# Kernel tuning notes

Hardware: AMD Instinct MI355X
Metric: run time of the kernel (lower is better)

The kernel has to match this reference:

```python
import jax, jax.numpy as jnp
import numpy as np

H = 512        # num_hidden
Z = 512        # latent_len
TIME = 0.2
N_STEPS = 4    # fixed-step RK4 replaces adaptive dopri5 (same dynamics math)
B, N = 4, 4096


def _linear_params(k, fin, fout):
    k1, k2 = jax.random.split(k)
    s = 1.0 / np.sqrt(fin)
    W = jax.random.uniform(k1, (fout, fin), minval=-s, maxval=s, dtype=jnp.float32)
    b = jax.random.uniform(k2, (fout,), minval=-s, maxval=s, dtype=jnp.float32)
    return W, b


def setup_inputs() -> dict:
    key = jax.random.key(0)
    ks = jax.random.split(key, 16)
    inp = {
        "code": jax.random.normal(ks[0], (B, 1, Z), dtype=jnp.float32),
        "x": jax.random.uniform(ks[1], (B, N, 3), dtype=jnp.float32),
    }
    dims = {"l1": (3, H), "l2": (H, H), "l3": (H, H), "l4": (H, 3), "cond": (Z, H)}
    i = 2
    for f in ("f1", "f2"):
        for name, (fin, fout) in dims.items():
            W, b = _linear_params(ks[i], fin, fout)
            i += 1
            inp[f + "_" + name + "_w"] = W
            inp[f + "_" + name + "_b"] = b
    return inp


def _node_block(x, sf, W1, b1, W2, b2, W3, b3, W4, b4):
    """Fixed-step RK4 integration of ODEFunc dynamics over [0, TIME].
    x: (B,N,3) point state; sf: (B,1,H) precomputed tanh(cond(code)) shape features
    (constant along the trajectory since the latent code has zero dynamics)."""
    def dyn(p):
        pf = jax.nn.relu(p @ W1.T + b1)          # (B,N,H) point features
        h = pf * sf                               # gated point-shape features
        h = jax.nn.relu(h @ W2.T + b2) + h        # residual stage 1
        h = jax.nn.relu(h @ W3.T + b3) + h        # residual stage 2
        return jnp.tanh(h @ W4.T + b4)            # (B,N,3) flow direction

    dt = TIME / N_STEPS
    def step(p, _):
        k1 = dyn(p)
        k2 = dyn(p + 0.5 * dt * k1)
        k3 = dyn(p + 0.5 * dt * k2)
        k4 = dyn(p + dt * k3)
        return p + (dt / 6.0) * (k1 + 2.0 * k2 + 2.0 * k3 + k4), None

    x, _ = jax.lax.scan(step, x, None, length=N_STEPS)
    return x


def reference(code, x,
              f1_l1_w, f1_l1_b, f1_l2_w, f1_l2_b, f1_l3_w, f1_l3_b,
              f1_l4_w, f1_l4_b, f1_cond_w, f1_cond_b,
              f2_l1_w, f2_l1_b, f2_l2_w, f2_l2_b, f2_l3_w, f2_l3_b,
              f2_l4_w, f2_l4_b, f2_cond_w, f2_cond_b):
    sf1 = jnp.tanh(code @ f1_cond_w.T + f1_cond_b)  # (B,1,H), broadcasts over N
    x = _node_block(x, sf1, f1_l1_w, f1_l1_b, f1_l2_w, f1_l2_b,
                    f1_l3_w, f1_l3_b, f1_l4_w, f1_l4_b)
    sf2 = jnp.tanh(code @ f2_cond_w.T + f2_cond_b)
    x = _node_block(x, sf2, f2_l1_w, f2_l1_b, f2_l2_w, f2_l2_b,
                    f2_l3_w, f2_l3_b, f2_l4_w, f2_l4_b)
    return x  # pred_y: (B,N,3)
```

## Files before the change

### kernel.cpp

```cpp
#include <hip/hip_runtime.h>
#include <stdint.h>

typedef short short8 __attribute__((ext_vector_type(8)));
typedef float floatx16 __attribute__((ext_vector_type(16)));

#define NPTS 16384
#define TILE_M 64
#define THREADS 512
#define PA 4
#define PB 8

__device__ inline unsigned short f2bf(float f) {
  union { float f; unsigned u; } v; v.f = f;
  unsigned u = v.u;
  unsigned r = (u + 0x7fffu + ((u >> 16) & 1u)) >> 16;
  return (unsigned short)r;
}
__device__ inline float bf2f(unsigned short h) {
  union { unsigned u; float f; } v; v.u = ((unsigned)h) << 16;
  return v.f;
}

__global__ __launch_bounds__(THREADS, 2) void dyn_kernel(
    const float* __restrict__ p, const float* __restrict__ kprev, float cf,
    const unsigned short* __restrict__ w2f, const unsigned short* __restrict__ w3f,
    const float* __restrict__ sf, const float* __restrict__ w1,
    const float* __restrict__ b1, const float* __restrict__ b2,
    const float* __restrict__ b3, const float* __restrict__ w4,
    const float* __restrict__ b4, int update_mode, float* __restrict__ outp,
    const float* __restrict__ k1v, const float* __restrict__ k2v,
    const float* __restrict__ k3v, float dt6)
{
  __shared__ unsigned short act[TILE_M][520];
  __shared__ float pe[TILE_M][3];
  __shared__ float red[192][8];

  const int tid = threadIdx.x;
  const int wg = blockIdx.x;
  const int m0 = wg * TILE_M;
  const int batch = wg >> 6;
  const int lane = tid & 63;
  const int wid = tid >> 6;

  if (tid < TILE_M * 3) {
    int gi = m0 * 3 + tid;
    ((float*)pe)[tid] = p[gi] + cf * kprev[gi];
  }
  __syncthreads();

  {
    int j = tid;
    float ww0 = w1[j * 3 + 0], ww1 = w1[j * 3 + 1], ww2 = w1[j * 3 + 2];
    float bb = b1[j];
    float s = sf[batch * 512 + j];
    #pragma unroll 4
    for (int m = 0; m < TILE_M; ++m) {
      float v = fmaf(pe[m][0], ww0, fmaf(pe[m][1], ww1, fmaf(pe[m][2], ww2, bb)));
      v = fmaxf(v, 0.f) * s;
      act[m][j] = f2bf(v);
    }
  }
  __syncthreads();

  const int aBase = (lane & 31) * 1040 + (lane >> 5) * 16;
  const char* actB = (const char*)&act[0][0];
  const int bcol0 = (wid * 2 + 0) * 64 + lane;
  const int bcol1 = (wid * 2 + 1) * 64 + lane;

  for (int s = 0; s < 2; ++s) {
    const short8* bptr = (const short8*)(s ? w3f : w2f);
    const float* bias = s ? b3 : b2;
    const short8* bp0 = bptr + bcol0;
    const short8* bp1 = bptr + bcol1;
    floatx16 acc00{}, acc01{}, acc10{}, acc11{};

    short8 aq0[PA], aq1[PA], bq0[PB], bq1[PB];
    #pragma unroll
    for (int i = 0; i < PB - 1; ++i) {
      bq0[i] = bp0[i * 1024];
      bq1[i] = bp1[i * 1024];
    }
    #pragma unroll
    for (int i = 0; i < PA - 1; ++i) {
      aq0[i] = *(const short8*)(actB + aBase + i * 32);
      aq1[i] = *(const short8*)(actB + aBase + 33280 + i * 32);
    }

    #pragma unroll
    for (int kt = 0; kt < 32; ++kt) {
      int la = kt + PA - 1;
      if (la < 32) {
        aq0[la % PA] = *(const short8*)(actB + aBase + la * 32);
        aq1[la % PA] = *(const short8*)(actB + aBase + 33280 + la * 32);
      }
      int lb = kt + PB - 1;
      if (lb < 32) {
        bq0[lb % PB] = bp0[lb * 1024];
        bq1[lb % PB] = bp1[lb * 1024];
      }
      acc00 = __builtin_amdgcn_mfma_f32_32x32x16_bf16(aq0[kt % PA], bq0[kt % PB], acc00, 0, 0, 0);
      acc01 = __builtin_amdgcn_mfma_f32_32x32x16_bf16(aq0[kt % PA], bq1[kt % PB], acc01, 0, 0, 0);
      acc10 = __builtin_amdgcn_mfma_f32_32x32x16_bf16(aq1[kt % PA], bq0[kt % PB], acc10, 0, 0, 0);
      acc11 = __builtin_amdgcn_mfma_f32_32x32x16_bf16(aq1[kt % PA], bq1[kt % PB], acc11, 0, 0, 0);
    }

    __syncthreads();
    {
      int ncol0 = (wid * 2 + 0) * 32 + (lane & 31);
      int ncol1 = (wid * 2 + 1) * 32 + (lane & 31);
      float bs0 = bias[ncol0], bs1 = bias[ncol1];
      int rbase = 4 * (lane >> 5);
      #pragma unroll
      for (int reg = 0; reg < 16; ++reg) {
        int row = (reg & 3) + 8 * (reg >> 2) + rbase;
        float v = fmaxf(acc00[reg] + bs0, 0.f) + bf2f(act[row][ncol0]);
        act[row][ncol0] = f2bf(v);
        v = fmaxf(acc01[reg] + bs1, 0.f) + bf2f(act[row][ncol1]);
        act[row][ncol1] = f2bf(v);
        v = fmaxf(acc10[reg] + bs0, 0.f) + bf2f(act[32 + row][ncol0]);
        act[32 + row][ncol0] = f2bf(v);
        v = fmaxf(acc11[reg] + bs1, 0.f) + bf2f(act[32 + row][ncol1]);
        act[32 + row][ncol1] = f2bf(v);
      }
    }
    __syncthreads();
  }

  {
    int m = tid >> 3, jj = tid & 7;
    const unsigned short* arow = &act[m][0];
    float s0 = 0.f, s1 = 0.f, s2 = 0.f;
    #pragma unroll 8
    for (int kk = 0; kk < 64; ++kk) {
      int k = kk * 8 + jj;
      float a = bf2f(arow[k]);
      s0 = fmaf(a, w4[k], s0);
      s1 = fmaf(a, w4[512 + k], s1);
      s2 = fmaf(a, w4[1024 + k], s2);
    }
    red[m * 3 + 0][jj] = s0;
    red[m * 3 + 1][jj] = s1;
    red[m * 3 + 2][jj] = s2;
  }
  __syncthreads();
  if (tid < 192) {
    int mm = tid / 3, cc = tid % 3;
    float ssum = 0.f;
    #pragma unroll
    for (int q = 0; q < 8; ++q) ssum += red[tid][q];
    float flow = tanhf(ssum + b4[cc]);
    int gi = (m0 + mm) * 3 + cc;
    if (update_mode) {
      outp[gi] = p[gi] + dt6 * (k1v[gi] + 2.f * k2v[gi] + 2.f * k3v[gi] + flow);
    } else {
      outp[gi] = flow;
    }
  }
}

__global__ void setup_shuffle(const float* s0, const float* s1, const float* s2,
                              const float* s3, unsigned short* dst) {
  int idx = blockIdx.x * blockDim.x + threadIdx.x;
  int w = idx >> 15;
  int r = idx & 32767;
  int lane = r & 63;
  int tile = r >> 6;
  int nt = tile & 15, kt = tile >> 4;
  const float* W = (w == 0) ? s0 : (w == 1) ? s1 : (w == 2) ? s2 : s3;
  int n = nt * 32 + (lane & 31);
  int k0 = kt * 16 + (lane >> 5) * 8;
  const float* src = W + n * 512 + k0;
  unsigned short* d = dst + ((size_t)w << 18) + (size_t)r * 8;
  #pragma unroll
  for (int j = 0; j < 8; ++j) d[j] = f2bf(src[j]);
}

__global__ void setup_copy(const float* x, float* p) {
  int i = blockIdx.x * blockDim.x + threadIdx.x;
  if (i < NPTS * 3) p[i] = x[i];
}

__global__ void setup_sf(const float* code, const float* cw1, const float* cb1,
                         const float* cw2, const float* cb2, float* sfout) {
  int f = blockIdx.x >> 2, b = blockIdx.x & 3;
  const float* cw = f ? cw2 : cw1;
  const float* cb = f ? cb2 : cb1;
  int j = threadIdx.x;
  const float* c = code + b * 512;
  float s = cb[j];
  for (int k = 0; k < 512; ++k) s = fmaf(c[k], cw[j * 512 + k], s);
  sfout[f * 2048 + b * 512 + j] = tanhf(s);
}

extern "C" void kernel_launch(void* const* d_in, const int* in_sizes, int n_in,
                              void* d_out, int out_size, void* d_ws, size_t ws_size,
                              hipStream_t stream) {
  const float* code = (const float*)d_in[0];
  const float* x    = (const float*)d_in[1];
  char* ws = (char*)d_ws;
  float* p  = (float*)(ws);
  float* k1 = (float*)(ws + 196608);
  float* k2 = (float*)(ws + 2 * 196608);
  float* k3 = (float*)(ws + 3 * 196608);
  float* sf = (float*)(ws + 4 * 196608);
  unsigned short* wbf = (unsigned short*)(ws + 4 * 196608 + 16384);

  setup_shuffle<<<512, 256, 0, stream>>>((const float*)d_in[4], (const float*)d_in[6],
                                         (const float*)d_in[14], (const float*)d_in[16], wbf);
  setup_copy<<<192, 256, 0, stream>>>(x, p);
  setup_sf<<<8, 512, 0, stream>>>(code, (const float*)d_in[10], (const float*)d_in[11],
                                  (const float*)d_in[20], (const float*)d_in[21], sf);

  const float dt = 0.05f, dt6 = dt / 6.0f;
  float* out = (float*)d_out;
  for (int f = 0; f < 2; ++f) {
    const float* w1 = (const float*)d_in[2 + f * 10];
    const float* b1 = (const float*)d_in[3 + f * 10];
    const float* b2 = (const float*)d_in[5 + f * 10];
    const float* b3 = (const float*)d_in[7 + f * 10];
    const float* w4 = (const float*)d_in[8 + f * 10];
    const float* b4 = (const float*)d_in[9 + f * 10];
    const unsigned short* w2b = wbf + (f * 2 + 0) * 262144;
    const unsigned short* w3b = wbf + (f * 2 + 1) * 262144;
    const float* sff = sf + f * 2048;
    for (int st = 0; st < 4; ++st) {
      int last = (f == 1 && st == 3);
      dyn_kernel<<<256, THREADS, 0, stream>>>(p, p,  0.0f,      w2b, w3b, sff, w1, b1, b2, b3, w4, b4,
                                              0, k1, p, p, p, dt6);
      dyn_kernel<<<256, THREADS, 0, stream>>>(p, k1, 0.5f * dt, w2b, w3b, sff, w1, b1, b2, b3, w4, b4,
                                              0, k2, p, p, p, dt6);
      dyn_kernel<<<256, THREADS, 0, stream>>>(p, k2, 0.5f * dt, w2b, w3b, sff, w1, b1, b2, b3, w4, b4,
                                              0, k3, p, p, p, dt6);
      dyn_kernel<<<256, THREADS, 0, stream>>>(p, k3, dt,        w2b, w3b, sff, w1, b1, b2, b3, w4, b4,
                                              1, last ? out : p, k1, k2, k3, dt6);
    }
  }
}
```

Baseline: 942.6 us.

## Fuse all RK4 stages and both ODE blocks into one persistent kernel

Replaces the 32 per-stage kernel launches with a single kernel in which each workgroup keeps its 64-point tile's state, RK4 accumulator and stage input in shared memory and loops over both blocks, 4 steps and 4 stages. It also prefetches W2 fragments before the first-layer compute and replaces the shared-memory reduction for the output layer with wave shuffles. This removes launch overhead and the global round trips for p and k1..k3. The cost is that the grid stays at 256 workgroups for the whole run, so there is no inter-kernel overlap, and register pressure rises.

```diff
diff --git a/kernel.cpp b/kernel.cpp
--- a/kernel.cpp
+++ b/kernel.cpp
@@ -21,19 +21,20 @@
   return v.f;
 }
 
-__global__ __launch_bounds__(THREADS, 2) void dyn_kernel(
-    const float* __restrict__ p, const float* __restrict__ kprev, float cf,
-    const unsigned short* __restrict__ w2f, const unsigned short* __restrict__ w3f,
-    const float* __restrict__ sf, const float* __restrict__ w1,
-    const float* __restrict__ b1, const float* __restrict__ b2,
-    const float* __restrict__ b3, const float* __restrict__ w4,
-    const float* __restrict__ b4, int update_mode, float* __restrict__ outp,
-    const float* __restrict__ k1v, const float* __restrict__ k2v,
-    const float* __restrict__ k3v, float dt6)
+__global__ __launch_bounds__(THREADS, 2) void node_kernel(
+    const float* __restrict__ x, float* __restrict__ outp,
+    const unsigned short* __restrict__ wbf, const float* __restrict__ sfall,
+    const float* __restrict__ w1a, const float* __restrict__ b1a,
+    const float* __restrict__ b2a, const float* __restrict__ b3a,
+    const float* __restrict__ w4a, const float* __restrict__ b4a,
+    const float* __restrict__ w1b, const float* __restrict__ b1b,
+    const float* __restrict__ b2b, const float* __restrict__ b3b,
+    const float* __restrict__ w4b, const float* __restrict__ b4b)
 {
   __shared__ unsigned short act[TILE_M][520];
-  __shared__ float pe[TILE_M][3];
-  __shared__ float red[192][8];
+  __shared__ float pcur[TILE_M][3];
+  __shared__ float pev[TILE_M][3];
+  __shared__ float kac[TILE_M][3];
 
   const int tid = threadIdx.x;
   const int wg = blockIdx.x;
@@ -43,22 +44,9 @@
   const int wid = tid >> 6;
 
   if (tid < TILE_M * 3) {
-    int gi = m0 * 3 + tid;
-    ((float*)pe)[tid] = p[gi] + cf * kprev[gi];
-  }
-  __syncthreads();
-
-  {
-    int j = tid;
-    float ww0 = w1[j * 3 + 0], ww1 = w1[j * 3 + 1], ww2 = w1[j * 3 + 2];
-    float bb = b1[j];
-    float s = sf[batch * 512 + j];
-    #pragma unroll 4
-    for (int m = 0; m < TILE_M; ++m) {
-      float v = fmaf(pe[m][0], ww0, fmaf(pe[m][1], ww1, fmaf(pe[m][2], ww2, bb)));
-      v = fmaxf(v, 0.f) * s;
-      act[m][j] = f2bf(v);
-    }
+    float v = x[m0 * 3 + tid];
+    ((float*)pcur)[tid] = v;
+    ((float*)pev)[tid] = v;
   }
   __syncthreads();
 
@@ -67,95 +55,146 @@
   const int bcol0 = (wid * 2 + 0) * 64 + lane;
   const int bcol1 = (wid * 2 + 1) * 64 + lane;
 
-  for (int s = 0; s < 2; ++s) {
-    const short8* bptr = (const short8*)(s ? w3f : w2f);
-    const float* bias = s ? b3 : b2;
-    const short8* bp0 = bptr + bcol0;
-    const short8* bp1 = bptr + bcol1;
-    floatx16 acc00{}, acc01{}, acc10{}, acc11{};
-
-    short8 aq0[PA], aq1[PA], bq0[PB], bq1[PB];
-    #pragma unroll
-    for (int i = 0; i < PB - 1; ++i) {
-      bq0[i] = bp0[i * 1024];
-      bq1[i] = bp1[i * 1024];
-    }
-    #pragma unroll
-    for (int i = 0; i < PA - 1; ++i) {
-      aq0[i] = *(const short8*)(actB + aBase + i * 32);
-      aq1[i] = *(const short8*)(actB + aBase + 33280 + i * 32);
-    }
-
-    #pragma unroll
-    for (int kt = 0; kt < 32; ++kt) {
-      int la = kt + PA - 1;
-      if (la < 32) {
-        aq0[la % PA] = *(const short8*)(actB + aBase + la * 32);
-        aq1[la % PA] = *(const short8*)(actB + aBase + 33280 + la * 32);
-      }
-      int lb = kt + PB - 1;
-      if (lb < 32) {
-        bq0[lb % PB] = bp0[lb * 1024];
-        bq1[lb % PB] = bp1[lb * 1024];
-      }
-      acc00 = __builtin_amdgcn_mfma_f32_32x32x16_bf16(aq0[kt % PA], bq0[kt % PB], acc00, 0, 0, 0);
-      acc01 = __builtin_amdgcn_mfma_f32_32x32x16_bf16(aq0[kt % PA], bq1[kt % PB], acc01, 0, 0, 0);
-      acc10 = __builtin_amdgcn_mfma_f32_32x32x16_bf16(aq1[kt % PA], bq0[kt % PB], acc10, 0, 0, 0);
-      acc11 = __builtin_amdgcn_mfma_f32_32x32x16_bf16(aq1[kt % PA], bq1[kt % PB], acc11, 0, 0, 0);
-    }
-
-    __syncthreads();
-    {
-      int ncol0 = (wid * 2 + 0) * 32 + (lane & 31);
-      int ncol1 = (wid * 2 + 1) * 32 + (lane & 31);
-      float bs0 = bias[ncol0], bs1 = bias[ncol1];
-      int rbase = 4 * (lane >> 5);
-      #pragma unroll
-      for (int reg = 0; reg < 16; ++reg) {
-        int row = (reg & 3) + 8 * (reg >> 2) + rbase;
-        float v = fmaxf(acc00[reg] + bs0, 0.f) + bf2f(act[row][ncol0]);
-        act[row][ncol0] = f2bf(v);
-        v = fmaxf(acc01[reg] + bs1, 0.f) + bf2f(act[row][ncol1]);
-        act[row][ncol1] = f2bf(v);
-        v = fmaxf(acc10[reg] + bs0, 0.f) + bf2f(act[32 + row][ncol0]);
-        act[32 + row][ncol0] = f2bf(v);
-        v = fmaxf(acc11[reg] + bs1, 0.f) + bf2f(act[32 + row][ncol1]);
-        act[32 + row][ncol1] = f2bf(v);
+  const float dt = 0.05f;
+
+  #pragma unroll 1
+  for (int f = 0; f < 2; ++f) {
+    const float* w1 = f ? w1b : w1a;
+    const float* b1v = f ? b1b : b1a;
+    const float* b2v = f ? b2b : b2a;
+    const float* b3v = f ? b3b : b3a;
+    const float* w4 = f ? w4b : w4a;
+    const float* b4v = f ? b4b : b4a;
+    const short8* w2p0 = (const short8*)(wbf + (size_t)(f * 2 + 0) * 262144) + bcol0;
+    const short8* w2p1 = (const short8*)(wbf + (size_t)(f * 2 + 0) * 262144) + bcol1;
+    const short8* w3p0 = (const short8*)(wbf + (size_t)(f * 2 + 1) * 262144) + bcol0;
+    const short8* w3p1 = (const short8*)(wbf + (size_t)(f * 2 + 1) * 262144) + bcol1;
+
+    const float ww0 = w1[tid * 3 + 0], ww1 = w1[tid * 3 + 1], ww2 = w1[tid * 3 + 2];
+    const float bb = b1v[tid];
+    const float ss = sfall[f * 2048 + batch * 512 + tid];
+    const float b40 = b4v[0], b41 = b4v[1], b42 = b4v[2];
+
+    #pragma unroll 1
+    for (int st = 0; st < 4; ++st) {
+      #pragma unroll 1
+      for (int stage = 0; stage < 4; ++stage) {
+        short8 bq0[PB], bq1[PB];
+        #pragma unroll
+        for (int i = 0; i < PB - 1; ++i) {
+          bq0[i] = w2p0[i * 1024];
+          bq1[i] = w2p1[i * 1024];
+        }
+
+        #pragma unroll 4
+        for (int m = 0; m < TILE_M; ++m) {
+          float v = fmaf(pev[m][0], ww0, fmaf(pev[m][1], ww1, fmaf(pev[m][2], ww2, bb)));
+          v = fmaxf(v, 0.f) * ss;
+          act[m][tid] = f2bf(v);
+        }
+        __syncthreads();
+
+        for (int s = 0; s < 2; ++s) {
+          const short8* bp0 = s ? w3p0 : w2p0;
+          const short8* bp1 = s ? w3p1 : w2p1;
+          const float* bias = s ? b3v : b2v;
+          floatx16 acc00{}, acc01{}, acc10{}, acc11{};
+          short8 aq0[PA], aq1[PA];
+          if (s == 1) {
+            #pragma unroll
+            for (int i = 0; i < PB - 1; ++i) {
+              bq0[i] = bp0[i * 1024];
+              bq1[i] = bp1[i * 1024];
+            }
+          }
+          #pragma unroll
+          for (int i = 0; i < PA - 1; ++i) {
+            aq0[i] = *(const short8*)(actB + aBase + i * 32);
+            aq1[i] = *(const short8*)(actB + aBase + 33280 + i * 32);
+          }
+
+          #pragma unroll
+          for (int kt = 0; kt < 32; ++kt) {
+            int la = kt + PA - 1;
+            if (la < 32) {
+              aq0[la % PA] = *(const short8*)(actB + aBase + la * 32);
+              aq1[la % PA] = *(const short8*)(actB + aBase + 33280 + la * 32);
+            }
+            int lb = kt + PB - 1;
+            if (lb < 32) {
+              bq0[lb % PB] = bp0[lb * 1024];
+              bq1[lb % PB] = bp1[lb * 1024];
+            }
+            acc00 = __builtin_amdgcn_mfma_f32_32x32x16_bf16(aq0[kt % PA], bq0[kt % PB], acc00, 0, 0, 0);
+            acc01 = __builtin_amdgcn_mfma_f32_32x32x16_bf16(aq0[kt % PA], bq1[kt % PB], acc01, 0, 0, 0);
+            acc10 = __builtin_amdgcn_mfma_f32_32x32x16_bf16(aq1[kt % PA], bq0[kt % PB], acc10, 0, 0, 0);
+            acc11 = __builtin_amdgcn_mfma_f32_32x32x16_bf16(aq1[kt % PA], bq1[kt % PB], acc11, 0, 0, 0);
+          }
+
+          __syncthreads();
+          {
+            int ncol0 = (wid * 2 + 0) * 32 + (lane & 31);
+            int ncol1 = (wid * 2 + 1) * 32 + (lane & 31);
+            float bs0 = bias[ncol0], bs1 = bias[ncol1];
+            int rbase = 4 * (lane >> 5);
+            #pragma unroll
+            for (int reg = 0; reg < 16; ++reg) {
+              int row = (reg & 3) + 8 * (reg >> 2) + rbase;
+              float v = fmaxf(acc00[reg] + bs0, 0.f) + bf2f(act[row][ncol0]);
+              act[row][ncol0] = f2bf(v);
+              v = fmaxf(acc01[reg] + bs1, 0.f) + bf2f(act[row][ncol1]);
+              act[row][ncol1] = f2bf(v);
+              v = fmaxf(acc10[reg] + bs0, 0.f) + bf2f(act[32 + row][ncol0]);
+              act[32 + row][ncol0] = f2bf(v);
+              v = fmaxf(acc11[reg] + bs1, 0.f) + bf2f(act[32 + row][ncol1]);
+              act[32 + row][ncol1] = f2bf(v);
+            }
+          }
+          __syncthreads();
+        }
+
+        {
+          int m = tid >> 3, jj = tid & 7;
+          const unsigned short* arow = &act[m][0];
+          float s0 = 0.f, s1 = 0.f, s2 = 0.f;
+          #pragma unroll 8
+          for (int kk = 0; kk < 64; ++kk) {
+            int k = kk * 8 + jj;
+            float a = bf2f(arow[k]);
+            s0 = fmaf(a, w4[k], s0);
+            s1 = fmaf(a, w4[512 + k], s1);
+            s2 = fmaf(a, w4[1024 + k], s2);
+          }
+          s0 += __shfl_xor(s0, 1); s1 += __shfl_xor(s1, 1); s2 += __shfl_xor(s2, 1);
+          s0 += __shfl_xor(s0, 2); s1 += __shfl_xor(s1, 2); s2 += __shfl_xor(s2, 2);
+          s0 += __shfl_xor(s0, 4); s1 += __shfl_xor(s1, 4); s2 += __shfl_xor(s2, 4);
+          if (jj < 3) {
+            float sv = (jj == 0) ? s0 : ((jj == 1) ? s1 : s2);
+            float bv = (jj == 0) ? b40 : ((jj == 1) ? b41 : b42);
+            float fl = tanhf(sv + bv);
+            float pc = pcur[m][jj];
+            if (stage == 0) {
+              kac[m][jj] = fl;
+              pev[m][jj] = fmaf(0.5f * dt, fl, pc);
+            } else if (stage == 1) {
+              kac[m][jj] += 2.f * fl;
+              pev[m][jj] = fmaf(0.5f * dt, fl, pc);
+            } else if (stage == 2) {
+              kac[m][jj] += 2.f * fl;
+              pev[m][jj] = fmaf(dt, fl, pc);
+            } else {
+              float np = fmaf(dt / 6.f, kac[m][jj] + fl, pc);
+              pcur[m][jj] = np;
+              pev[m][jj] = np;
+            }
+          }
+        }
+        __syncthreads();
       }
     }
-    __syncthreads();
   }
 
-  {
-    int m = tid >> 3, jj = tid & 7;
-    const unsigned short* arow = &act[m][0];
-    float s0 = 0.f, s1 = 0.f, s2 = 0.f;
-    #pragma unroll 8
-    for (int kk = 0; kk < 64; ++kk) {
-      int k = kk * 8 + jj;
-      float a = bf2f(arow[k]);
-      s0 = fmaf(a, w4[k], s0);
-      s1 = fmaf(a, w4[512 + k], s1);
-      s2 = fmaf(a, w4[1024 + k], s2);
-    }
-    red[m * 3 + 0][jj] = s0;
-    red[m * 3 + 1][jj] = s1;
-    red[m * 3 + 2][jj] = s2;
-  }
-  __syncthreads();
-  if (tid < 192) {
-    int mm = tid / 3, cc = tid % 3;
-    float ssum = 0.f;
-    #pragma unroll
-    for (int q = 0; q < 8; ++q) ssum += red[tid][q];
-    float flow = tanhf(ssum + b4[cc]);
-    int gi = (m0 + mm) * 3 + cc;
-    if (update_mode) {
-      outp[gi] = p[gi] + dt6 * (k1v[gi] + 2.f * k2v[gi] + 2.f * k3v[gi] + flow);
-    } else {
-      outp[gi] = flow;
-    }
-  }
+  if (tid < TILE_M * 3) outp[m0 * 3 + tid] = ((const float*)pcur)[tid];
 }
 
 __global__ void setup_shuffle(const float* s0, const float* s1, const float* s2,
@@ -175,11 +214,6 @@
   for (int j = 0; j < 8; ++j) d[j] = f2bf(src[j]);
 }
 
-__global__ void setup_copy(const float* x, float* p) {
-  int i = blockIdx.x * blockDim.x + threadIdx.x;
-  if (i < NPTS * 3) p[i] = x[i];
-}
-
 __global__ void setup_sf(const float* code, const float* cw1, const float* cb1,
                          const float* cw2, const float* cb2, float* sfout) {
   int f = blockIdx.x >> 2, b = blockIdx.x & 3;
@@ -198,41 +232,17 @@
   const float* code = (const float*)d_in[0];
   const float* x    = (const float*)d_in[1];
   char* ws = (char*)d_ws;
-  float* p  = (float*)(ws);
-  float* k1 = (float*)(ws + 196608);
-  float* k2 = (float*)(ws + 2 * 196608);
-  float* k3 = (float*)(ws + 3 * 196608);
-  float* sf = (float*)(ws + 4 * 196608);
-  unsigned short* wbf = (unsigned short*)(ws + 4 * 196608 + 16384);
+  float* sf = (float*)ws;
+  unsigned short* wbf = (unsigned short*)(ws + 16384);
 
   setup_shuffle<<<512, 256, 0, stream>>>((const float*)d_in[4], (const float*)d_in[6],
                                          (const float*)d_in[14], (const float*)d_in[16], wbf);
-  setup_copy<<<192, 256, 0, stream>>>(x, p);
   setup_sf<<<8, 512, 0, stream>>>(code, (const float*)d_in[10], (const float*)d_in[11],
                                   (const float*)d_in[20], (const float*)d_in[21], sf);
 
-  const float dt = 0.05f, dt6 = dt / 6.0f;
-  float* out = (float*)d_out;
-  for (int f = 0; f < 2; ++f) {
-    const float* w1 = (const float*)d_in[2 + f * 10];
-    const float* b1 = (const float*)d_in[3 + f * 10];
-    const float* b2 = (const float*)d_in[5 + f * 10];
-    const float* b3 = (const float*)d_in[7 + f * 10];
-    const float* w4 = (const float*)d_in[8 + f * 10];
-    const float* b4 = (const float*)d_in[9 + f * 10];
-    const unsigned short* w2b = wbf + (f * 2 + 0) * 262144;
-    const unsigned short* w3b = wbf + (f * 2 + 1) * 262144;
-    const float* sff = sf + f * 2048;
-    for (int st = 0; st < 4; ++st) {
-      int last = (f == 1 && st == 3);
-      dyn_kernel<<<256, THREADS, 0, stream>>>(p, p,  0.0f,      w2b, w3b, sff, w1, b1, b2, b3, w4, b4,
-                                              0, k1, p, p, p, dt6);
-      dyn_kernel<<<256, THREADS, 0, stream>>>(p, k1, 0.5f * dt, w2b, w3b, sff, w1, b1, b2, b3, w4, b4,
-                                              0, k2, p, p, p, dt6);
-      dyn_kernel<<<256, THREADS, 0, stream>>>(p, k2, 0.5f * dt, w2b, w3b, sff, w1, b1, b2, b3, w4, b4,
-                                              0, k3, p, p, p, dt6);
-      dyn_kernel<<<256, THREADS, 0, stream>>>(p, k3, dt,        w2b, w3b, sff, w1, b1, b2, b3, w4, b4,
-                                              1, last ? out : p, k1, k2, k3, dt6);
-    }
-  }
-}
+  node_kernel<<<256, THREADS, 0, stream>>>(x, (float*)d_out, wbf, sf,
+      (const float*)d_in[2], (const float*)d_in[3], (const float*)d_in[5],
+      (const float*)d_in[7], (const float*)d_in[8], (const float*)d_in[9],
+      (const float*)d_in[12], (const float*)d_in[13], (const float*)d_in[15],
+      (const float*)d_in[17], (const float*)d_in[18], (const float*)d_in[19]);
+}
```

After: 923.1 us. 2.1% less time.
